# Performance work log

Hardware: AMD Instinct MI355X
Metric: run time of the kernel (lower is better)

The kernel has to match this reference:

```python
import jax, jax.numpy as jnp
import numpy as np

TEMPERATURE = 1.0
STRIDE = 1
PADDING = 2
RF = 5  # receptive_field_size
TREE_DEPTH = 3

# Each of the 16 binary difflogic ops op_g(a,b) is multilinear:
# op_g = c0 + c1*a + c2*b + c3*a*b. Rows ordered per the standard difflogic table:
# 0:0, 1:a&b, 2:a&~b, 3:a, 4:~a&b, 5:b, 6:xor, 7:or, 8:nor, 9:xnor,
# 10:~b, 11:a|~b, 12:~a, 13:~a|b, 14:nand, 15:1
_C = jnp.asarray(np.array([
    [0, 0, 0, 0],
    [0, 0, 0, 1],
    [0, 1, 0, -1],
    [0, 1, 0, 0],
    [0, 0, 1, -1],
    [0, 0, 1, 0],
    [0, 1, 1, -2],
    [0, 1, 1, -1],
    [1, -1, -1, 1],
    [1, -1, -1, 2],
    [1, 0, -1, 0],
    [1, 0, -1, 1],
    [1, -1, 0, 0],
    [1, -1, 0, 1],
    [1, 0, 0, -1],
    [1, 0, 0, 0]], dtype=np.float32))


def _gate(a, b, logits):
    """Soft LUT gate. a,b: (B,K,N,P); logits: (N,K,16) -> (B,K,N,P)."""
    w = jax.nn.softmax(logits / TEMPERATURE, axis=-1)          # (N,K,16)
    coef = jnp.einsum('nkg,gc->knc', w, _C)                    # (K,N,4)
    c = coef[None, :, :, None, :]                              # (1,K,N,1,4)
    return c[..., 0] + c[..., 1] * a + c[..., 2] * b + c[..., 3] * (a * b)


def setup_inputs() -> dict:
    key = jax.random.key(0)
    ks = jax.random.split(key, 8)
    B, Cin, H, W = 16, 32, 64, 64
    K, N = 64, 2 ** TREE_DEPTH  # num_kernels, leaf gates per tree
    x = jax.random.uniform(ks[0], (B, Cin, H, W), dtype=jnp.float32)
    idx_h = jax.random.randint(ks[1], (2, K, N), 0, RF, dtype=jnp.int32)
    idx_w = jax.random.randint(ks[2], (2, K, N), 0, RF, dtype=jnp.int32)
    idx_c = jax.random.randint(ks[3], (2, K, N), 0, Cin, dtype=jnp.int32)
    w0 = jax.random.normal(ks[4], (8, K, 16), dtype=jnp.float32)
    w1 = jax.random.normal(ks[5], (4, K, 16), dtype=jnp.float32)
    w2 = jax.random.normal(ks[6], (2, K, 16), dtype=jnp.float32)
    w3 = jax.random.normal(ks[7], (1, K, 16), dtype=jnp.float32)
    return {"x": x, "idx_h": idx_h, "idx_w": idx_w, "idx_c": idx_c,
            "w0": w0, "w1": w1, "w2": w2, "w3": w3}


def reference(x, idx_h, idx_w, idx_c, w0, w1, w2, w3):
    B, Cin, H, W = x.shape
    xp = jnp.pad(x, ((0, 0), (0, 0), (PADDING, PADDING), (PADDING, PADDING)))
    out_h = (H + 2 * PADDING - RF) // STRIDE + 1
    out_w = (W + 2 * PADDING - RF) // STRIDE + 1
    # Absolute gather coords per (rank-slot, kernel, leaf-gate, out_y, out_x)
    abs_h = idx_h[..., None, None] + (jnp.arange(out_h) * STRIDE)[:, None]   # (2,K,N,oh,1)
    abs_w = idx_w[..., None, None] + (jnp.arange(out_w) * STRIDE)[None, :]   # (2,K,N,1,ow)
    cc = idx_c[..., None, None]                                              # (2,K,N,1,1)
    g = xp[:, cc, abs_h, abs_w]                                # (B,2,K,N,oh,ow)
    K, N = g.shape[2], g.shape[3]
    g = g.reshape(B, 2, K, N, out_h * out_w)                   # (B,2,K,N,P)
    cur = _gate(g[:, 0], g[:, 1], w0)                          # (B,K,8,P) leaf level
    for wl in (w1, w2, w3):                                    # reduce tree: 8->4->2->1
        cur = _gate(cur[:, :, 0::2, :], cur[:, :, 1::2, :], wl)
    return cur.reshape(B, K, out_h, out_w)
```

## Files before the change

kernel.cpp:

```cpp
#include <hip/hip_runtime.h>
#include <hip/hip_bf16.h>

#define CIN 32
#define HW 64
#define KK 64
#define NLEAF 8
#define PADDING 2
#define TH 4
#define TCW 16
#define WR 8
#define WC 20
#define WPOS (CIN * WR * WC)

typedef float f32x2 __attribute__((ext_vector_type(2)));

__device__ __constant__ float d_C[16][4] = {
    {0, 0, 0, 0},  {0, 0, 0, 1},  {0, 1, 0, -1}, {0, 1, 0, 0},
    {0, 0, 1, -1}, {0, 0, 1, 0},  {0, 1, 1, -2}, {0, 1, 1, -1},
    {1, -1, -1, 1},{1, -1, -1, 2},{1, 0, -1, 0}, {1, 0, -1, 1},
    {1, -1, 0, 0}, {1, -1, 0, 1}, {1, 0, 0, -1}, {1, 0, 0, 0}
};

__global__ __launch_bounds__(256) void prep_kernel(
    const int* __restrict__ idx_h, const int* __restrict__ idx_w, const int* __restrict__ idx_c,
    const float* __restrict__ w0, const float* __restrict__ w1,
    const float* __restrict__ w2, const float* __restrict__ w3,
    float* __restrict__ coefA, int* __restrict__ loffA)
{
    int tid = blockIdx.x * 256 + threadIdx.x;

    {
        int k = tid >> 4, n = tid & 15;
        int s = n >> 3, leaf = n & 7;
        int o = s * (KK * NLEAF) + k * NLEAF + leaf;
        loffA[tid] = (idx_c[o] * (WR * WC) + idx_h[o] * WC + idx_w[o]) * 8;
    }

    if (tid < KK * 15) {
        int k = tid / 15, node = tid % 15;
        const float* wp; int n;
        if (node < 8)       { wp = w0; n = node; }
        else if (node < 12) { wp = w1; n = node - 8; }
        else if (node < 14) { wp = w2; n = node - 12; }
        else                { wp = w3; n = 0; }
        const float4* lp = (const float4*)(wp + (size_t)(n * KK + k) * 16);
        float4 L0 = lp[0], L1 = lp[1], L2 = lp[2], L3 = lp[3];
        float l[16] = {L0.x, L0.y, L0.z, L0.w, L1.x, L1.y, L1.z, L1.w,
                       L2.x, L2.y, L2.z, L2.w, L3.x, L3.y, L3.z, L3.w};
        float m = l[0];
        #pragma unroll
        for (int g = 1; g < 16; ++g) m = fmaxf(m, l[g]);
        float p[16], s = 0.f;
        #pragma unroll
        for (int g = 0; g < 16; ++g) { p[g] = __expf(l[g] - m); s += p[g]; }
        float inv = 1.f / s;
        float c0 = 0, c1 = 0, c2 = 0, c3 = 0;
        #pragma unroll
        for (int g = 0; g < 16; ++g) {
            float w = p[g] * inv;
            c0 = fmaf(w, d_C[g][0], c0);
            c1 = fmaf(w, d_C[g][1], c1);
            c2 = fmaf(w, d_C[g][2], c2);
            c3 = fmaf(w, d_C[g][3], c3);
        }
        float* o = coefA + (k * 60 + node * 4);
        o[0] = c0; o[1] = c1; o[2] = c2; o[3] = c3;
    }
}

__device__ __forceinline__ f32x2 bc(float s) { return (f32x2){s, s}; }
__device__ __forceinline__ f32x2 gate2(const float* c, f32x2 a, f32x2 b) {
    return __builtin_elementwise_fma(b,
               __builtin_elementwise_fma(a, bc(c[3]), bc(c[2])),
               __builtin_elementwise_fma(a, bc(c[1]), bc(c[0])));
}

__global__ __launch_bounds__(512) void logic_conv_kernel(
    const float* __restrict__ x, const int* __restrict__ loffA,
    const float* __restrict__ coefA, float* __restrict__ out)
{
    __shared__ f32x2 xt[WPOS];

    int tid = threadIdx.x;
    int bp  = blockIdx.x & 7;
    int t   = blockIdx.x >> 3;
    int r0  = (t >> 2) * TH;
    int c0  = (t & 3) * TCW;

    int lane = tid & 63, wave = tid >> 6;
    int kbase = __builtin_amdgcn_readfirstlane(wave << 3);
    int tr = lane >> 4, tc = lane & 15;
    int pxb = (tr * WC + tc) * 8;

    int ga[8][16];
    #pragma unroll
    for (int j = 0; j < 8; ++j) {
        const int* L = loffA + ((kbase + j) << 4);
        #pragma unroll
        for (int n = 0; n < 16; ++n)
            ga[j][n] = L[n] + pxb;
    }

    const float* xb0 = x + (size_t)(2 * bp) * (CIN * HW * HW);
    const float* xb1 = xb0 + (CIN * HW * HW);

    #pragma unroll
    for (int i = 0; i < 10; ++i) {
        int e  = tid + i * 512;
        int c  = e / (WR * WC);
        int r  = e - c * (WR * WC);
        int rr = r / WC;
        int cc = r - rr * WC;
        int ih = r0 + rr - PADDING, iw = c0 + cc - PADDING;
        f32x2 v = {0.f, 0.f};
        if ((unsigned)ih < HW && (unsigned)iw < HW) {
            int go = (c * HW + ih) * HW + iw;
            v.x = xb0[go];
            v.y = xb1[go];
        }
        xt[e] = v;
    }
    __syncthreads();

    int pxout = (r0 + tr) * HW + (c0 + tc);
    float* outB0 = out + ((size_t)(2 * bp) << 18);
    float* outB1 = outB0 + (1 << 18);
    const char* xtb = (const char*)xt;

    #pragma unroll
    for (int j = 0; j < 8; ++j) {
        const float* C = coefA + (kbase + j) * 60;

        f32x2 g[16];
        #pragma unroll
        for (int n = 0; n < 16; ++n)
            g[n] = *(const f32x2*)(xtb + ga[j][n]);

        f32x2 v[8];
        #pragma unroll
        for (int n = 0; n < 8; ++n)
            v[n] = gate2(C + 4 * n, g[n], g[8 + n]);
        f32x2 u[4];
        #pragma unroll
        for (int n = 0; n < 4; ++n)
            u[n] = gate2(C + 32 + 4 * n, v[2 * n], v[2 * n + 1]);
        f32x2 t0 = gate2(C + 48, u[0], u[1]);
        f32x2 t1 = gate2(C + 52, u[2], u[3]);
        f32x2 r  = gate2(C + 56, t0, t1);

        int ko = ((kbase + j) << 12) + pxout;
        __builtin_nontemporal_store(r.x, &outB0[ko]);
        __builtin_nontemporal_store(r.y, &outB1[ko]);
    }
}

extern "C" void kernel_launch(void* const* d_in, const int* in_sizes, int n_in,
                              void* d_out, int out_size, void* d_ws, size_t ws_size,
                              hipStream_t stream) {
    const float* x     = (const float*)d_in[0];
    const int*   idx_h = (const int*)d_in[1];
    const int*   idx_w = (const int*)d_in[2];
    const int*   idx_c = (const int*)d_in[3];
    const float* w0    = (const float*)d_in[4];
    const float* w1    = (const float*)d_in[5];
    const float* w2    = (const float*)d_in[6];
    const float* w3    = (const float*)d_in[7];
    float* out   = (float*)d_out;

    float* coefA = (float*)d_ws;
    int*   loffA = (int*)((char*)d_ws + 16384);

    hipLaunchKernelGGL(prep_kernel, dim3(4), dim3(256), 0, stream,
                       idx_h, idx_w, idx_c, w0, w1, w2, w3, coefA, loffA);
    hipLaunchKernelGGL(logic_conv_kernel, dim3(512), dim3(512), 0, stream,
                       x, loffA, coefA, out);
}
```

Baseline: 25.16 us.

## Split kernels across blocks and double-buffer two column tiles per block

Each block now handles half the kernels (32 instead of 64) for two adjacent column tiles. The second tile's global loads are issued into registers while the first tile is computed from shared memory, then stored into a second LDS buffer. Gather offsets become wave-uniform scalars via readfirstlane instead of per-lane registers, which cuts VGPR pressure, and launch bounds request 4 blocks per CU. The cost is doubled LDS per block (80KB), which may limit residency, and each block loads its input window once per kernel half, so input loads are duplicated.

```diff
diff --git a/kernel.cpp b/kernel.cpp
--- a/kernel.cpp
+++ b/kernel.cpp
@@ -75,35 +75,41 @@
                __builtin_elementwise_fma(a, bc(c[1]), bc(c[0])));
 }
 
-__global__ __launch_bounds__(512) void logic_conv_kernel(
+__global__ __launch_bounds__(512, 4) void logic_conv_kernel(
     const float* __restrict__ x, const int* __restrict__ loffA,
     const float* __restrict__ coefA, float* __restrict__ out)
 {
-    __shared__ f32x2 xt[WPOS];
+    __shared__ f32x2 xt[2][WPOS];
 
     int tid = threadIdx.x;
     int bp  = blockIdx.x & 7;
-    int t   = blockIdx.x >> 3;
-    int r0  = (t >> 2) * TH;
-    int c0  = (t & 3) * TCW;
+    int rem = blockIdx.x >> 3;
+    int kh  = rem & 1;
+    int tp  = rem >> 1;
+    int t0  = tp * 2;
+    int r0  = (t0 >> 2) * TH;
+    int c00 = (t0 & 3) * TCW;
+    int c01 = c00 + TCW;
 
     int lane = tid & 63, wave = tid >> 6;
-    int kbase = __builtin_amdgcn_readfirstlane(wave << 3);
+    int kbase = __builtin_amdgcn_readfirstlane(kh * 32 + wave * 4);
     int tr = lane >> 4, tc = lane & 15;
     int pxb = (tr * WC + tc) * 8;
 
-    int ga[8][16];
-    #pragma unroll
-    for (int j = 0; j < 8; ++j) {
-        const int* L = loffA + ((kbase + j) << 4);
+    int soff[4][16];
+    #pragma unroll
+    for (int j = 0; j < 4; ++j) {
         #pragma unroll
         for (int n = 0; n < 16; ++n)
-            ga[j][n] = L[n] + pxb;
+            soff[j][n] = __builtin_amdgcn_readfirstlane(
+                             loffA[((kbase + j) << 4) + n]);
     }
 
     const float* xb0 = x + (size_t)(2 * bp) * (CIN * HW * HW);
     const float* xb1 = xb0 + (CIN * HW * HW);
 
+    int sgo[10];
+    int siw[10];
     #pragma unroll
     for (int i = 0; i < 10; ++i) {
         int e  = tid + i * 512;
@@ -111,47 +117,72 @@
         int r  = e - c * (WR * WC);
         int rr = r / WC;
         int cc = r - rr * WC;
-        int ih = r0 + rr - PADDING, iw = c0 + cc - PADDING;
-        f32x2 v = {0.f, 0.f};
-        if ((unsigned)ih < HW && (unsigned)iw < HW) {
-            int go = (c * HW + ih) * HW + iw;
-            v.x = xb0[go];
-            v.y = xb1[go];
-        }
-        xt[e] = v;
-    }
-    __syncthreads();
-
-    int pxout = (r0 + tr) * HW + (c0 + tc);
+        int ih = r0 + rr - PADDING;
+        sgo[i] = ((unsigned)ih < HW) ? (c * HW + ih) * HW : -1;
+        siw[i] = cc - PADDING;
+    }
+
+#define LOADW(c0x, dst)                                                   \
+    {                                                                     \
+        _Pragma("unroll")                                                 \
+        for (int i = 0; i < 10; ++i) {                                    \
+            int iw = (c0x) + siw[i];                                      \
+            f32x2 v = {0.f, 0.f};                                         \
+            if (sgo[i] >= 0 && (unsigned)iw < HW) {                       \
+                int go = sgo[i] + iw;                                     \
+                v.x = xb0[go]; v.y = xb1[go];                             \
+            }                                                             \
+            dst[i] = v;                                                   \
+        }                                                                 \
+    }
+
     float* outB0 = out + ((size_t)(2 * bp) << 18);
     float* outB1 = outB0 + (1 << 18);
-    const char* xtb = (const char*)xt;
-
-    #pragma unroll
-    for (int j = 0; j < 8; ++j) {
-        const float* C = coefA + (kbase + j) * 60;
-
-        f32x2 g[16];
-        #pragma unroll
-        for (int n = 0; n < 16; ++n)
-            g[n] = *(const f32x2*)(xtb + ga[j][n]);
-
-        f32x2 v[8];
-        #pragma unroll
-        for (int n = 0; n < 8; ++n)
-            v[n] = gate2(C + 4 * n, g[n], g[8 + n]);
-        f32x2 u[4];
-        #pragma unroll
-        for (int n = 0; n < 4; ++n)
-            u[n] = gate2(C + 32 + 4 * n, v[2 * n], v[2 * n + 1]);
-        f32x2 t0 = gate2(C + 48, u[0], u[1]);
-        f32x2 t1 = gate2(C + 52, u[2], u[3]);
-        f32x2 r  = gate2(C + 56, t0, t1);
-
-        int ko = ((kbase + j) << 12) + pxout;
-        __builtin_nontemporal_store(r.x, &outB0[ko]);
-        __builtin_nontemporal_store(r.y, &outB1[ko]);
-    }
+
+#define COMPUTE(XTB, c0x)                                                 \
+    {                                                                     \
+        int pxout = (r0 + tr) * HW + ((c0x) + tc);                        \
+        _Pragma("unroll")                                                 \
+        for (int j = 0; j < 4; ++j) {                                     \
+            const float* C = coefA + (kbase + j) * 60;                    \
+            f32x2 g[16];                                                  \
+            _Pragma("unroll")                                             \
+            for (int n = 0; n < 16; ++n)                                  \
+                g[n] = *(const f32x2*)((XTB) + (soff[j][n] + pxb));       \
+            f32x2 v[8];                                                   \
+            _Pragma("unroll")                                             \
+            for (int n = 0; n < 8; ++n)                                   \
+                v[n] = gate2(C + 4 * n, g[n], g[8 + n]);                  \
+            f32x2 u[4];                                                   \
+            _Pragma("unroll")                                             \
+            for (int n = 0; n < 4; ++n)                                   \
+                u[n] = gate2(C + 32 + 4 * n, v[2 * n], v[2 * n + 1]);     \
+            f32x2 q0 = gate2(C + 48, u[0], u[1]);                         \
+            f32x2 q1 = gate2(C + 52, u[2], u[3]);                         \
+            f32x2 rr2 = gate2(C + 56, q0, q1);                            \
+            int ko = ((kbase + j) << 12) + pxout;                         \
+            __builtin_nontemporal_store(rr2.x, &outB0[ko]);               \
+            __builtin_nontemporal_store(rr2.y, &outB1[ko]);               \
+        }                                                                 \
+    }
+
+    f32x2 sv[10];
+    LOADW(c00, sv);
+    #pragma unroll
+    for (int i = 0; i < 10; ++i) xt[0][tid + i * 512] = sv[i];
+    __syncthreads();
+
+    LOADW(c01, sv);
+
+    COMPUTE((const char*)&xt[0][0], c00);
+
+    #pragma unroll
+    for (int i = 0; i < 10; ++i) xt[1][tid + i * 512] = sv[i];
+    __syncthreads();
+    COMPUTE((const char*)&xt[1][0], c01);
+
+#undef LOADW
+#undef COMPUTE
 }
 
 extern "C" void kernel_launch(void* const* d_in, const int* in_sizes, int n_in,
```

Result: slower. 28.18 us (+12.0%).
